# Optimization experiments

Hardware: AMD Instinct MI355X
Metric: run time of the kernel (lower is better)

## Reference

```python
import jax, jax.numpy as jnp
import numpy as np

B, N = 2, 6
C_IN, C_MID = 512, 512
D, C_OUT = 112, 80
OGH, OGW, DS = 256, 704, 16
FH, FW = OGH // DS, OGW // DS  # 16, 44
D_MIN, D_MAX = 2.0, 58.0
NX, NY, NZ = 128, 128, 1
VSIZE = np.array([0.8, 0.8, 8.0], dtype=np.float32)
VCOORD = np.array([-51.2 + 0.4, -51.2 + 0.4, -5.0 + 4.0], dtype=np.float32)


def make_frustum():
    # (D, FH, FW, 4) with entries (x_pix, y_pix, depth, 1)
    ones = jnp.ones((D, FH, FW), jnp.float32)
    d = jnp.linspace(D_MIN, D_MAX, D)[:, None, None] * jnp.ones((1, FH, FW))
    x = jnp.linspace(0.0, OGW - 1.0, FW)[None, None, :] * jnp.ones((D, FH, 1))
    y = jnp.linspace(0.0, OGH - 1.0, FH)[None, :, None] * jnp.ones((D, 1, FW))
    return jnp.stack([x, y, d, ones], axis=-1)


def setup_inputs() -> dict:
    key = jax.random.key(0)
    ks = jax.random.split(key, 24)
    eye = jnp.eye(4, dtype=jnp.float32)
    K = jnp.array([[1266.0, 0.0, 800.0, 0.0],
                   [0.0, 1266.0, 450.0, 0.0],
                   [0.0, 0.0, 1.0, 0.0],
                   [0.0, 0.0, 0.0, 1.0]], jnp.float32)
    inp = {
        'feat': jax.random.normal(ks[0], (B * N, C_IN, FH, FW), jnp.float32),
        'w1': 0.05 * jax.random.normal(ks[1], (C_MID, C_IN, 3, 3), jnp.float32),
        'g1': 1.0 + 0.1 * jax.random.normal(ks[2], (C_MID,), jnp.float32),
        'b1': 0.1 * jax.random.normal(ks[3], (C_MID,), jnp.float32),
        'm1': 0.1 * jax.random.normal(ks[4], (C_MID,), jnp.float32),
        'v1': 0.5 + jax.random.uniform(ks[5], (C_MID,), jnp.float32),
        'w2': 0.05 * jax.random.normal(ks[6], (C_MID, C_MID, 3, 3), jnp.float32),
        'g2': 1.0 + 0.1 * jax.random.normal(ks[7], (C_MID,), jnp.float32),
        'b2': 0.1 * jax.random.normal(ks[8], (C_MID,), jnp.float32),
        'm2': 0.1 * jax.random.normal(ks[9], (C_MID,), jnp.float32),
        'v2': 0.5 + jax.random.uniform(ks[10], (C_MID,), jnp.float32),
        'w_out': 0.05 * jax.random.normal(ks[11], (D + C_OUT, C_MID, 1, 1), jnp.float32),
        'b_out': 0.1 * jax.random.normal(ks[12], (D + C_OUT,), jnp.float32),
        'sensor2ego': eye + 0.05 * jax.random.normal(ks[13], (B, N, 4, 4), jnp.float32),
        'sensor2virtual': eye + 0.05 * jax.random.normal(ks[14], (B, N, 4, 4), jnp.float32),
        'intrin': K + 0.01 * jax.random.normal(ks[15], (B, N, 4, 4), jnp.float32),
        'ida': eye + 0.01 * jax.random.normal(ks[16], (B, N, 4, 4), jnp.float32),
        'ref_heights': 1.5 + 0.2 * jax.random.normal(ks[17], (B, N), jnp.float32),
        'bda': eye + 0.01 * jax.random.normal(ks[18], (B, 4, 4), jnp.float32),
    }
    return inp


def _conv(x, w, p):
    return jax.lax.conv_general_dilated(x, w, (1, 1), [(p, p), (p, p)],
                                         dimension_numbers=('NCHW', 'OIHW', 'NCHW'))


def _bn(x, g, b, m, v):
    s = (g / jnp.sqrt(v + 1e-5))
    return (x - m[None, :, None, None]) * s[None, :, None, None] + b[None, :, None, None]


def get_geometry(sensor2ego, sensor2virtual, intrin, ida, ref_heights, bda):
    frustum = make_frustum()[..., None]  # (D,FH,FW,4,1)
    pts = jnp.linalg.inv(ida)[:, :, None, None, None] @ frustum  # (B,N,D,FH,FW,4,1)
    ref = ref_heights[:, :, None, None, None, None]
    height = -pts[..., 2, :] + ref  # (B,N,D,FH,FW,1)
    pc = pts.at[..., 2, :].set(10.0)
    pc = jnp.concatenate([pc[..., :2, :] * pc[..., 2:3, :], pc[..., 2:, :]], axis=-2)
    cv = sensor2virtual @ jnp.linalg.inv(intrin)
    pv = cv[:, :, None, None, None] @ pc
    ratio = height[..., 0] / pv[..., 1, 0]  # (B,N,D,FH,FW)
    pts = pv * ratio[..., None, None]
    pts = pts.at[..., 3, :].set(1.0)
    ce = sensor2ego @ jnp.linalg.inv(sensor2virtual)
    pts = ce[:, :, None, None, None] @ pts
    pts = (bda[:, None, None, None, None] @ pts)[..., 0]
    return pts[..., :3]  # (B,N,D,FH,FW,3)


def reference(feat, w1, g1, b1, m1, v1, w2, g2, b2, m2, v2, w_out, b_out,
              sensor2ego, sensor2virtual, intrin, ida, ref_heights, bda):
    # DepthNet head
    h = jax.nn.relu(_bn(_conv(feat, w1, 1), g1, b1, m1, v1))
    h = jax.nn.relu(_bn(_conv(h, w2, 1), g2, b2, m2, v2))
    hf = _conv(h, w_out, 0) + b_out[None, :, None, None]  # (B*N, D+C, FH, FW)
    depth = jax.nn.softmax(hf[:, :D], axis=1).reshape(B, N, D, FH, FW)
    context = hf[:, D:].reshape(B, N, C_OUT, FH, FW)

    geom = get_geometry(sensor2ego, sensor2virtual, intrin, ida, ref_heights, bda)

    # voxel indices
    vsize = jnp.asarray(VSIZE)
    vcoord = jnp.asarray(VCOORD)
    idx = ((geom - (vcoord - vsize / 2.0)) / vsize).astype(jnp.int32)
    valid = (jnp.all(idx >= 0, axis=-1) & (idx[..., 0] < NX)
             & (idx[..., 1] < NY) & (idx[..., 2] < NZ))

    # LSS outer product: (B,N,D,FH,FW,C)
    vol = jnp.einsum('bndhw,bnchw->bndhwc', depth, context)
    YX = NY * NX
    sid = idx[..., 1] * NX + idx[..., 0] + jnp.arange(B, dtype=jnp.int32)[:, None, None, None, None] * YX
    sid = jnp.where(valid, sid, B * YX).reshape(-1)
    bev = jax.ops.segment_sum(vol.reshape(-1, C_OUT), sid, num_segments=B * YX + 1)[:B * YX]
    return bev.reshape(B, NY, NX, C_OUT).transpose(0, 3, 1, 2)  # (B,C,NY,NX)
```

## Files before the change

kernel.cpp:

```cpp
#include <hip/hip_runtime.h>
#include <stdint.h>

#define NB   2
#define NN   6
#define NIMG 12
#define CIN  512
#define CMID 512
#define DD   112
#define COUT 80
#define FHh  16
#define FWw  44
#define NPIX 704
#define NPOS 8448
#define KK   4608
#define NXg  128
#define NYg  128
#define YX   16384
#define MAT_STRIDE 56
#define PADPIX 828
#define PROW 46
#define KSPLIT 4
#define KCHUNK (KK/KSPLIT)
#define NSTEP (KCHUNK/32)

typedef short short8 __attribute__((ext_vector_type(8)));
typedef float f32x4  __attribute__((ext_vector_type(4)));

#define GLD16(g, l) __builtin_amdgcn_global_load_lds((const __attribute__((address_space(1))) void*)(g), (__attribute__((address_space(3))) void*)(l), 16, 0, 0)

__device__ __forceinline__ unsigned short f2bf(float f){
  unsigned u = __float_as_uint(f);
  u += 0x7fffu + ((u >> 16) & 1u);
  return (unsigned short)(u >> 16);
}
__device__ __forceinline__ float bf2f(unsigned short u){
  return __uint_as_float(((unsigned)u) << 16);
}

__device__ __forceinline__ f32x4 mfma16(short8 a, short8 b, f32x4 c){
  return __builtin_amdgcn_mfma_f32_16x16x32_bf16(a, b, c, 0, 0, 0);
}

#define N1 (CMID*KK)
__global__ void k_prep_misc(const float* __restrict__ w1, const float* __restrict__ w2,
                            const float* __restrict__ wout,
                            const float* __restrict__ g1, const float* __restrict__ b1,
                            const float* __restrict__ m1, const float* __restrict__ v1,
                            const float* __restrict__ g2, const float* __restrict__ b2,
                            const float* __restrict__ m2, const float* __restrict__ v2,
                            unsigned short* __restrict__ wb1, unsigned short* __restrict__ wb2,
                            unsigned short* __restrict__ wb3,
                            float* __restrict__ scale1, float* __restrict__ bias1,
                            float* __restrict__ scale2, float* __restrict__ bias2){
  int i = blockIdx.x*blockDim.x + threadIdx.x;
  if (i < 2*N1){
    const float* w = (i < N1) ? w1 : w2;
    unsigned short* wb = (i < N1) ? wb1 : wb2;
    int j = (i < N1) ? i : i - N1;
    int oc = j / KK; int jj = j - oc*KK;
    int r = jj >> 9; int ic = jj & 511;
    wb[j] = f2bf(w[(size_t)(oc*512 + ic)*9 + r]);
  } else if (i < 2*N1 + 192*CMID){
    int j = i - 2*N1;
    wb3[j] = f2bf(wout[j]);
  } else if (i < 2*N1 + 192*CMID + 512){
    int t = i - (2*N1 + 192*CMID);
    float s = g1[t] / sqrtf(v1[t] + 1e-5f);
    scale1[t] = s; bias1[t] = b1[t] - m1[t]*s;
  } else if (i < 2*N1 + 192*CMID + 1024){
    int t = i - (2*N1 + 192*CMID + 512);
    float s = g2[t] / sqrtf(v2[t] + 1e-5f);
    scale2[t] = s; bias2[t] = b2[t] - m2[t]*s;
  }
}

__global__ void k_zeropad(unsigned short* __restrict__ a, unsigned short* __restrict__ b,
                          float4* __restrict__ bev){
  int i = blockIdx.x*blockDim.x + threadIdx.x;
  if (i < NB*YX*COUT/4) bev[i] = make_float4(0.f,0.f,0.f,0.f);
  int img = i >> 16; int j = i & 65535;
  int seg = j >> 9, ch = j & 511;
  int pp;
  if (seg < 46)       pp = seg;
  else if (seg < 92)  pp = 17*PROW + (seg - 46);
  else { int s2 = seg - 92; int y = s2 >> 1; pp = y*PROW + ((s2 & 1) ? 45 : 0); }
  size_t off = (size_t)img*PADPIX*512 + (size_t)pp*512 + ch;
  a[off] = 0; b[off] = 0;
}

__global__ __launch_bounds__(256) void k_featpad(const float* __restrict__ feat,
                                                 unsigned short* __restrict__ dst){
  __shared__ float tile[32][65];
  int blk = blockIdx.x;
  int img = blk / 176; int r = blk - img*176;
  int cb = r / 11; int pb = r - cb*11;
  int c0 = cb*32, p0 = pb*64;
  int t = threadIdx.x;
  const float* s = feat + (size_t)img*CIN*NPIX + (size_t)c0*NPIX + p0;
  for (int ch = t>>6; ch < 32; ch += 4)
    tile[ch][t & 63] = s[(size_t)ch*NPIX + (t & 63)];
  __syncthreads();
  int ch = (t & 15)*2;
  for (int pix = t>>4; pix < 64; pix += 16){
    int p = p0 + pix;
    int y = p / FWw, x = p - y*FWw;
    unsigned v = (unsigned)f2bf(tile[ch][pix]) | ((unsigned)f2bf(tile[ch+1][pix]) << 16);
    *(unsigned*)(dst + (size_t)img*PADPIX*512 + ((y+1)*PROW + (x+1))*512 + c0 + ch) = v;
  }
}

__device__ void inv4(const double* A, double* out){
  double M[4][8];
  for (int i=0;i<4;i++){ for(int j=0;j<4;j++){ M[i][j]=A[i*4+j]; M[i][4+j]=(i==j)?1.0:0.0; } }
  for (int c=0;c<4;c++){
    int piv=c; double best=fabs(M[c][c]);
    for (int r=c+1;r<4;r++){ double a=fabs(M[r][c]); if(a>best){best=a;piv=r;} }
    if (piv!=c){ for(int j=0;j<8;j++){ double tt=M[c][j]; M[c][j]=M[piv][j]; M[piv][j]=tt; } }
    double inv = 1.0 / M[c][c];
    for (int j=0;j<8;j++) M[c][j]*=inv;
    for (int r=0;r<4;r++){ if(r==c) continue; double f=M[r][c];
      for (int j=0;j<8;j++) M[r][j]-=f*M[c][j]; }
  }
  for (int i=0;i<4;i++) for(int j=0;j<4;j++) out[i*4+j]=M[i][4+j];
}
__device__ void mm4(const double* A, const double* Bm, double* C){
  for (int i=0;i<4;i++) for(int j=0;j<4;j++){
    double s=0.0; for(int k=0;k<4;k++) s+=A[i*4+k]*Bm[k*4+j]; C[i*4+j]=s; }
}

__global__ void k_prep_mats(const float* __restrict__ s2e, const float* __restrict__ s2v,
                            const float* __restrict__ intr, const float* __restrict__ ida,
                            const float* __restrict__ refh, const float* __restrict__ bda,
                            double* __restrict__ mats){
  int t = threadIdx.x;
  if (t >= NIMG) return;
  int b = t / NN;
  double Mida[16], Ms2v[16], Mintr[16], Ms2e[16], Mbda[16];
  for (int i=0;i<16;i++){
    Mida[i] =(double)ida [t*16+i];
    Ms2v[i] =(double)s2v [t*16+i];
    Mintr[i]=(double)intr[t*16+i];
    Ms2e[i] =(double)s2e [t*16+i];
    Mbda[i] =(double)bda [b*16+i];
  }
  double* o = mats + (size_t)t*MAT_STRIDE;
  double tmp[16], tmp2[16];
  inv4(Mida, o);
  inv4(Mintr, tmp);  mm4(Ms2v, tmp, o+16);
  inv4(Ms2v, tmp);   mm4(Ms2e, tmp, tmp2);
  mm4(Mbda, tmp2, o+32);
  o[48] = (double)refh[t];
}

__global__ void k_geom(const double* __restrict__ mats, int* __restrict__ sid){
  int g = blockIdx.x*blockDim.x + threadIdx.x;
  int img = g / (DD*NPIX); int rem = g - img*(DD*NPIX);
  int d = rem / NPIX; int p = rem - d*NPIX;
  int h = p / FWw; int w = p - h*FWw;
  const double* M = mats + (size_t)img*MAT_STRIDE;
  float xf = (float)w * (703.0f/43.0f);
  float yf = (float)h * 17.0f;
  float df = 2.0f + (float)d * (56.0f/111.0f);
  double x = (double)xf, y = (double)yf, dep = (double)df;
  double p0 = M[0]*x + M[1]*y + M[2]*dep + M[3];
  double p1 = M[4]*x + M[5]*y + M[6]*dep + M[7];
  double p2 = M[8]*x + M[9]*y + M[10]*dep + M[11];
  double p3 = M[12]*x + M[13]*y + M[14]*dep + M[15];
  double height = M[48] - p2;
  double c0 = p0*10.0, c1 = p1*10.0, c2 = 10.0, c3 = p3;
  const double* C = M + 16;
  double q0 = C[0]*c0 + C[1]*c1 + C[2]*c2 + C[3]*c3;
  double q1 = C[4]*c0 + C[5]*c1 + C[6]*c2 + C[7]*c3;
  double q2 = C[8]*c0 + C[9]*c1 + C[10]*c2 + C[11]*c3;
  double ratio = height / q1;
  double r0 = q0*ratio, r1 = q1*ratio, r2 = q2*ratio, r3 = 1.0;
  const double* F = M + 32;
  double gx = F[0]*r0 + F[1]*r1 + F[2]*r2 + F[3]*r3;
  double gy = F[4]*r0 + F[5]*r1 + F[6]*r2 + F[7]*r3;
  double gz = F[8]*r0 + F[9]*r1 + F[10]*r2 + F[11]*r3;
  float gxf = (float)gx, gyf = (float)gy, gzf = (float)gz;
  const float vcx = (float)(-51.2 + 0.4);
  const float ox = vcx - 0.4f;
  const float oy = ox;
  const float oz = -1.0f - 4.0f;
  float tx = (gxf - ox) / 0.8f;
  float ty = (gyf - oy) / 0.8f;
  float tz = (gzf - oz) / 8.0f;
  int ix = (int)tx, iy = (int)ty, iz = (int)tz;
  bool valid = (tx==tx) && (ty==ty) && (tz==tz) &&
               (ix >= 0) && (ix < NXg) && (iy >= 0) && (iy < NYg) && (iz == 0);
  int b = img / NN;
  sid[g] = valid ? (b*YX + iy*NXg + ix) : -1;
}

__global__ __launch_bounds__(256, 4) void k_conv_sk(const unsigned short* __restrict__ W,
    const unsigned short* __restrict__ src, unsigned short* __restrict__ part){
  __shared__ __align__(16) short As[3][128*32];
  __shared__ __align__(16) short Bs[3][128*32];
  int t = threadIdx.x;
  int lane = t & 63, wv = t >> 6;
  int wm = wv >> 1, wn = wv & 1;
  int q = lane >> 4, ml = lane & 15;

  int id = blockIdx.x;
  int res = id & 7, slot = id >> 3;
  int g = res + 8*(slot >> 2);
  int mblk = slot & 3;
  int z = g / 66, n = g - z*66;
  int m0 = mblk*128, n0 = n*128, k0 = z*KCHUNK;

  int lrow = lane >> 2;
  int lcol = (lane & 3) * 8;
  const unsigned short* agp[2];
  const unsigned short* bgp[2];
  #pragma unroll
  for (int i=0;i<2;i++){
    int seg = wv*2 + i;
    agp[i] = W + (size_t)(m0 + seg*16 + lrow)*KK + lcol;
    int pos = n0 + seg*16 + lrow;
    int img = pos / NPIX; int p = pos - img*NPIX;
    int y = p / FWw; int x = p - y*FWw;
    bgp[i] = src + (size_t)img*PADPIX*512 + ((y+1)*PROW + (x+1))*512 + lcol;
  }

  f32x4 acc[4][4];
  #pragma unroll
  for (int i=0;i<4;i++)
    #pragma unroll
    for (int j=0;j<4;j++) acc[i][j] = (f32x4)0.0f;

  auto stage = [&](int step, int d){
    int kb = k0 + step*32;
    int r = kb >> 9;
    int ic0 = kb & 511;
    int r3 = r / 3;
    int koff = (r3*PROW + (r - r3*3))*512 + ic0 - (PROW+1)*512;
    #pragma unroll
    for (int i=0;i<2;i++){
      int seg = wv*2 + i;
      GLD16(agp[i] + kb,   (char*)As[d] + seg*1024);
      GLD16(bgp[i] + koff, (char*)Bs[d] + seg*1024);
    }
  };

  stage(0, 0); stage(1, 1);
  int d = 0;
  for (int k = 0; k < NSTEP; ++k){
    if (k < NSTEP-1) asm volatile("s_waitcnt vmcnt(4)" ::: "memory");
    else             asm volatile("s_waitcnt vmcnt(0)" ::: "memory");
    asm volatile("s_barrier" ::: "memory");
    if (k + 2 < NSTEP){
      int nxt = d + 2; if (nxt >= 3) nxt -= 3;
      stage(k + 2, nxt);
    }
    const short* Ab = As[d];
    const short* Bb = Bs[d];
    short8 fa[4], fb[4];
    #pragma unroll
    for (int mi=0;mi<4;mi++) fa[mi] = *(const short8*)(Ab + (wm*64 + mi*16 + ml)*32 + q*8);
    #pragma unroll
    for (int ni=0;ni<4;ni++) fb[ni] = *(const short8*)(Bb + (wn*64 + ni*16 + ml)*32 + q*8);
    #pragma unroll
    for (int mi=0;mi<4;mi++)
      #pragma unroll
      for (int ni=0;ni<4;ni++)
        acc[mi][ni] = mfma16(fb[ni], fa[mi], acc[mi][ni]);
    d = (d == 2) ? 0 : d + 1;
  }

  unsigned short* op = part + (size_t)z*NPOS*CMID;
  #pragma unroll
  for (int mi=0;mi<4;mi++){
    int oc = m0 + wm*64 + mi*16 + ml;
    #pragma unroll
    for (int ni=0;ni<4;ni++){
      f32x4 v = acc[mi][ni];
      #pragma unroll
      for (int rr=0;rr<4;rr++){
        int pos = n0 + wn*64 + ni*16 + q*4 + rr;
        op[(size_t)pos*CMID + oc] = f2bf(v[rr]);
      }
    }
  }
}

template<int OUT_PADDED>
__global__ void k_reduce(const unsigned short* __restrict__ part,
                         const float* __restrict__ scale, const float* __restrict__ bias,
                         unsigned short* __restrict__ out){
  int i2 = blockIdx.x*blockDim.x + threadIdx.x;
  int e0 = i2*2;
  const size_t S = (size_t)NPOS*CMID;
  unsigned p0 = *(const unsigned*)(part + e0);
  unsigned p1 = *(const unsigned*)(part + e0 + S);
  unsigned p2 = *(const unsigned*)(part + e0 + 2*S);
  unsigned p3 = *(const unsigned*)(part + e0 + 3*S);
  float s0 = bf2f((unsigned short)p0) + bf2f((unsigned short)p1)
           + bf2f((unsigned short)p2) + bf2f((unsigned short)p3);
  float s1 = bf2f((unsigned short)(p0>>16)) + bf2f((unsigned short)(p1>>16))
           + bf2f((unsigned short)(p2>>16)) + bf2f((unsigned short)(p3>>16));
  int pos = e0 >> 9, oc = e0 & 511;
  float v0 = fmaxf(s0*scale[oc]   + bias[oc],   0.0f);
  float v1 = fmaxf(s1*scale[oc+1] + bias[oc+1], 0.0f);
  unsigned packed = (unsigned)f2bf(v0) | ((unsigned)f2bf(v1) << 16);
  if (OUT_PADDED){
    int img = pos / NPIX; int p = pos - img*NPIX;
    int y = p / FWw; int x = p - y*FWw;
    *(unsigned*)(out + (size_t)img*PADPIX*512 + ((y+1)*PROW + (x+1))*512 + oc) = packed;
  } else {
    *(unsigned*)(out + e0) = packed;
  }
}

__global__ __launch_bounds__(256) void k_gemm64(const unsigned short* __restrict__ A,
    const unsigned short* __restrict__ Bt, const float* __restrict__ bout,
    float* __restrict__ hf){
  const int K = 512;
  __shared__ __align__(16) short As[64][32];
  __shared__ __align__(16) short Bs[128][32];
  int t = threadIdx.x;
  int m0 = blockIdx.x*64; int n0 = blockIdx.y*128;
  int lane = t & 63; int wv = t >> 6; int q = lane >> 4, ml = lane & 15;
  f32x4 acc[8];
  #pragma unroll
  for (int i=0;i<8;i++) acc[i] = (f32x4)0.0f;
  int ar = t >> 2, ac = (t & 3) * 8;
  int br = t >> 1, bc = (t & 1) * 16;
  const unsigned short* pa = A  + (size_t)(m0 + ar)*K + ac;
  const unsigned short* pb = Bt + (size_t)(n0 + br)*K + bc;
  for (int kb = 0; kb < K; kb += 32){
    uint4 av = *(const uint4*)(pa + kb);
    uint4 b0 = *(const uint4*)(pb + kb);
    uint4 b1 = *(const uint4*)(pb + kb + 8);
    __syncthreads();
    *(uint4*)&As[ar][ac] = av;
    *(uint4*)&Bs[br][bc] = b0; *(uint4*)&Bs[br][bc+8] = b1;
    __syncthreads();
    short8 fa = *(const short8*)&As[wv*16 + ml][q*8];
    #pragma unroll
    for (int ni=0;ni<8;ni++){
      short8 fb = *(const short8*)&Bs[ni*16 + ml][q*8];
      acc[ni] = mfma16(fb, fa, acc[ni]);
    }
  }
  int oc = m0 + wv*16 + ml;
  float bb = bout[oc];
  #pragma unroll
  for (int ni=0;ni<8;ni++)
    #pragma unroll
    for (int r=0;r<4;r++){
      int pos = n0 + ni*16 + q*4 + r;
      hf[(size_t)pos*192 + oc] = acc[ni][r] + bb;
    }
}

__global__ __launch_bounds__(128) void k_scatter(const float* __restrict__ hf,
                          const int* __restrict__ sidb, float* __restrict__ bev){
  int pos = blockIdx.x;
  int img = pos / NPIX; int p = pos - img*NPIX;
  __shared__ float sdep[DD];
  __shared__ int   ssid[DD];
  __shared__ float sctx[COUT];
  __shared__ float cwt[DD];
  __shared__ int   cvox[DD];
  __shared__ int   scnt;
  __shared__ float redm[2];
  __shared__ float reds[2];
  int t = threadIdx.x;
  int wv = t >> 6;
  if (t == 0) scnt = 0;
  const float* row = hf + (size_t)pos*192;
  float v = (t < DD) ? row[t] : -1e30f;
  for (int c = t; c < COUT; c += 128) sctx[c] = row[DD + c];
  if (t < DD) ssid[t] = sidb[(size_t)(img*DD + t)*NPIX + p];
  float m = v;
  #pragma unroll
  for (int o=32;o>=1;o>>=1) m = fmaxf(m, __shfl_xor(m, o, 64));
  if ((t & 63) == 0) redm[wv] = m;
  __syncthreads();
  float mx = fmaxf(redm[0], redm[1]);
  float e = (t < DD) ? __expf(v - mx) : 0.0f;
  float s = e;
  #pragma unroll
  for (int o=32;o>=1;o>>=1) s += __shfl_xor(s, o, 64);
  if ((t & 63) == 0) reds[wv] = s;
  __syncthreads();
  float inv = 1.0f / (reds[0] + reds[1]);
  if (t < DD) sdep[t] = e * inv;
  __syncthreads();
  if (t < DD){
    int sd = ssid[t];
    bool head = (sd >= 0) && (t == 0 || ssid[t-1] != sd);
    if (head){
      float w = 0.0f;
      for (int dd = t; dd < DD && ssid[dd] == sd; ++dd) w += sdep[dd];
      int i = atomicAdd(&scnt, 1);
      cvox[i] = sd; cwt[i] = w;
    }
  }
  __syncthreads();
  int H = scnt;
  for (int j = t; j < H*COUT; j += 128){
    int h = j / COUT, c = j - h*COUT;
    atomicAdd(&bev[(size_t)cvox[h]*COUT + c], cwt[h]*sctx[c]);
  }
}

__global__ __launch_bounds__(256) void k_transpose(const float* __restrict__ bev, float* __restrict__ out){
  __shared__ float tile[64*COUT];
  int blk = blockIdx.x;
  int b = blk >> 8; int yx0 = (blk & 255) * 64;
  int t = threadIdx.x;
  const float* src = bev + ((size_t)b*YX + yx0)*COUT;
  for (int j = t; j < 64*COUT; j += 256) tile[j] = src[j];
  __syncthreads();
  float* dst = out + (size_t)b*COUT*YX + yx0;
  for (int j = t; j < COUT*64; j += 256){
    int c = j >> 6, row = j & 63;
    dst[(size_t)c*YX + row] = tile[row*COUT + c];
  }
}

extern "C" void kernel_launch(void* const* d_in, const int* in_sizes, int n_in,
                              void* d_out, int out_size, void* d_ws, size_t ws_size,
                              hipStream_t stream) {
  const float* feat = (const float*)d_in[0];
  const float* w1   = (const float*)d_in[1];
  const float* g1   = (const float*)d_in[2];
  const float* b1   = (const float*)d_in[3];
  const float* m1   = (const float*)d_in[4];
  const float* v1   = (const float*)d_in[5];
  const float* w2   = (const float*)d_in[6];
  const float* g2   = (const float*)d_in[7];
  const float* b2   = (const float*)d_in[8];
  const float* m2   = (const float*)d_in[9];
  const float* v2   = (const float*)d_in[10];
  const float* wout = (const float*)d_in[11];
  const float* bout = (const float*)d_in[12];
  const float* s2e  = (const float*)d_in[13];
  const float* s2v  = (const float*)d_in[14];
  const float* intr = (const float*)d_in[15];
  const float* ida  = (const float*)d_in[16];
  const float* refh = (const float*)d_in[17];
  const float* bda  = (const float*)d_in[18];

  uint8_t* base = (uint8_t*)d_ws;
  size_t off = 0;
  auto alloc = [&](size_t bytes)->void*{
    void* r = base + off;
    off = (off + bytes + 255) & ~(size_t)255;
    return r;
  };
  unsigned short* wb1 = (unsigned short*)alloc((size_t)CMID*KK*2);
  unsigned short* wb2 = (unsigned short*)alloc((size_t)CMID*KK*2);
  unsigned short* wb3 = (unsigned short*)alloc((size_t)192*CMID*2);
  float* scale1 = (float*)alloc(CMID*4);
  float* bias1  = (float*)alloc(CMID*4);
  float* scale2 = (float*)alloc(CMID*4);
  float* bias2  = (float*)alloc(CMID*4);
  double* mats  = (double*)alloc((size_t)NIMG*MAT_STRIDE*8);

  size_t padded_bytes = (size_t)NIMG*PADPIX*512*2;
  uint8_t* regionE = (uint8_t*)alloc(padded_bytes);
  uint8_t* regionF = (uint8_t*)alloc(padded_bytes);
  int*   sid   = (int*)  alloc((size_t)NIMG*DD*NPIX*4);
  float* bev   = (float*)alloc((size_t)NB*YX*COUT*4);
  unsigned short* part = (unsigned short*)alloc((size_t)KSPLIT*NPOS*CMID*2);

  unsigned short* featpad = (unsigned short*)regionE;
  unsigned short* h2      = (unsigned short*)regionE;
  unsigned short* h1pad   = (unsigned short*)regionF;
  float*          hf      = (float*)regionF;

  int prep_n = 2*N1 + 192*CMID + 1024;
  k_prep_misc<<<(prep_n + 255)/256, 256, 0, stream>>>(w1, w2, wout, g1, b1, m1, v1,
      g2, b2, m2, v2, wb1, wb2, wb3, scale1, bias1, scale2, bias2);
  k_prep_mats<<<1, 64, 0, stream>>>(s2e, s2v, intr, ida, refh, bda, mats);
  k_geom<<<3696, 256, 0, stream>>>(mats, sid);

  k_zeropad<<<3072, 256, 0, stream>>>(featpad, h1pad, (float4*)bev);
  k_featpad<<<2112, 256, 0, stream>>>(feat, featpad);

  k_conv_sk<<<1056, 256, 0, stream>>>(wb1, featpad, part);
  k_reduce<1><<<NPOS*CMID/512, 256, 0, stream>>>(part, scale1, bias1, h1pad);
  k_conv_sk<<<1056, 256, 0, stream>>>(wb2, h1pad, part);
  k_reduce<0><<<NPOS*CMID/512, 256, 0, stream>>>(part, scale2, bias2, h2);
  k_gemm64<<<dim3(3, 66), 256, 0, stream>>>(wb3, h2, bout, hf);

  k_scatter<<<NPOS, 128, 0, stream>>>(hf, sid, bev);

  k_transpose<<<512, 256, 0, stream>>>(bev, (float*)d_out);
}
```

Measured before the change: 372.2 us.

## Raise conv split-K to 8 when workspace allows; double-buffer 1x1 GEMM with async LDS loads

```diff
diff --git a/kernel.cpp b/kernel.cpp
--- a/kernel.cpp
+++ b/kernel.cpp
@@ -19,9 +19,6 @@
 #define MAT_STRIDE 56
 #define PADPIX 828
 #define PROW 46
-#define KSPLIT 4
-#define KCHUNK (KK/KSPLIT)
-#define NSTEP (KCHUNK/32)
 
 typedef short short8 __attribute__((ext_vector_type(8)));
 typedef float f32x4  __attribute__((ext_vector_type(4)));
@@ -194,9 +191,10 @@
 }
 
 __global__ __launch_bounds__(256, 4) void k_conv_sk(const unsigned short* __restrict__ W,
-    const unsigned short* __restrict__ src, unsigned short* __restrict__ part){
-  __shared__ __align__(16) short As[3][128*32];
-  __shared__ __align__(16) short Bs[3][128*32];
+    const unsigned short* __restrict__ src, unsigned short* __restrict__ part,
+    int ksplit, int kchunk, int nstep){
+  __shared__ __align__(16) short As[2][128*32];
+  __shared__ __align__(16) short Bs[2][128*32];
   int t = threadIdx.x;
   int lane = t & 63, wv = t >> 6;
   int wm = wv >> 1, wn = wv & 1;
@@ -207,7 +205,7 @@
   int g = res + 8*(slot >> 2);
   int mblk = slot & 3;
   int z = g / 66, n = g - z*66;
-  int m0 = mblk*128, n0 = n*128, k0 = z*KCHUNK;
+  int m0 = mblk*128, n0 = n*128, k0 = z*kchunk;
 
   int lrow = lane >> 2;
   int lcol = (lane & 3) * 8;
@@ -229,8 +227,9 @@
     #pragma unroll
     for (int j=0;j<4;j++) acc[i][j] = (f32x4)0.0f;
 
-  auto stage = [&](int step, int d){
+  auto stage = [&](int step){
     int kb = k0 + step*32;
+    int d = step & 1;
     int r = kb >> 9;
     int ic0 = kb & 511;
     int r3 = r / 3;
@@ -243,18 +242,17 @@
     }
   };
 
-  stage(0, 0); stage(1, 1);
-  int d = 0;
-  for (int k = 0; k < NSTEP; ++k){
-    if (k < NSTEP-1) asm volatile("s_waitcnt vmcnt(4)" ::: "memory");
-    else             asm volatile("s_waitcnt vmcnt(0)" ::: "memory");
+  stage(0);
+  for (int k = 0; k < nstep; ++k){
+    if (k + 1 < nstep){
+      stage(k + 1);
+      asm volatile("s_waitcnt vmcnt(4)" ::: "memory");
+    } else {
+      asm volatile("s_waitcnt vmcnt(0)" ::: "memory");
+    }
     asm volatile("s_barrier" ::: "memory");
-    if (k + 2 < NSTEP){
-      int nxt = d + 2; if (nxt >= 3) nxt -= 3;
-      stage(k + 2, nxt);
-    }
-    const short* Ab = As[d];
-    const short* Bb = Bs[d];
+    const short* Ab = As[k & 1];
+    const short* Bb = Bs[k & 1];
     short8 fa[4], fb[4];
     #pragma unroll
     for (int mi=0;mi<4;mi++) fa[mi] = *(const short8*)(Ab + (wm*64 + mi*16 + ml)*32 + q*8);
@@ -265,7 +263,7 @@
       #pragma unroll
       for (int ni=0;ni<4;ni++)
         acc[mi][ni] = mfma16(fb[ni], fa[mi], acc[mi][ni]);
-    d = (d == 2) ? 0 : d + 1;
+    asm volatile("s_barrier" ::: "memory");
   }
 
   unsigned short* op = part + (size_t)z*NPOS*CMID;
@@ -287,18 +285,16 @@
 template<int OUT_PADDED>
 __global__ void k_reduce(const unsigned short* __restrict__ part,
                          const float* __restrict__ scale, const float* __restrict__ bias,
-                         unsigned short* __restrict__ out){
+                         unsigned short* __restrict__ out, int ksplit){
   int i2 = blockIdx.x*blockDim.x + threadIdx.x;
   int e0 = i2*2;
   const size_t S = (size_t)NPOS*CMID;
-  unsigned p0 = *(const unsigned*)(part + e0);
-  unsigned p1 = *(const unsigned*)(part + e0 + S);
-  unsigned p2 = *(const unsigned*)(part + e0 + 2*S);
-  unsigned p3 = *(const unsigned*)(part + e0 + 3*S);
-  float s0 = bf2f((unsigned short)p0) + bf2f((unsigned short)p1)
-           + bf2f((unsigned short)p2) + bf2f((unsigned short)p3);
-  float s1 = bf2f((unsigned short)(p0>>16)) + bf2f((unsigned short)(p1>>16))
-           + bf2f((unsigned short)(p2>>16)) + bf2f((unsigned short)(p3>>16));
+  float s0 = 0.0f, s1 = 0.0f;
+  for (int z = 0; z < ksplit; ++z){
+    unsigned pz = *(const unsigned*)(part + e0 + (size_t)z*S);
+    s0 += bf2f((unsigned short)pz);
+    s1 += bf2f((unsigned short)(pz >> 16));
+  }
   int pos = e0 >> 9, oc = e0 & 511;
   float v0 = fmaxf(s0*scale[oc]   + bias[oc],   0.0f);
   float v1 = fmaxf(s1*scale[oc+1] + bias[oc+1], 0.0f);
@@ -316,32 +312,48 @@
     const unsigned short* __restrict__ Bt, const float* __restrict__ bout,
     float* __restrict__ hf){
   const int K = 512;
-  __shared__ __align__(16) short As[64][32];
-  __shared__ __align__(16) short Bs[128][32];
+  __shared__ __align__(16) short As[2][64*32];
+  __shared__ __align__(16) short Bs[2][128*32];
   int t = threadIdx.x;
-  int m0 = blockIdx.x*64; int n0 = blockIdx.y*128;
-  int lane = t & 63; int wv = t >> 6; int q = lane >> 4, ml = lane & 15;
+  int lane = t & 63, wv = t >> 6;
+  int q = lane >> 4, ml = lane & 15;
+  int m0 = blockIdx.x*64, n0 = blockIdx.y*128;
+  int lrow = lane >> 2, lcol = (lane & 3) * 8;
+  const unsigned short* agp = A + (size_t)(m0 + wv*16 + lrow)*K + lcol;
+  const unsigned short* bgp[2];
+  #pragma unroll
+  for (int i=0;i<2;i++){
+    int seg = wv*2 + i;
+    bgp[i] = Bt + (size_t)(n0 + seg*16 + lrow)*K + lcol;
+  }
   f32x4 acc[8];
   #pragma unroll
   for (int i=0;i<8;i++) acc[i] = (f32x4)0.0f;
-  int ar = t >> 2, ac = (t & 3) * 8;
-  int br = t >> 1, bc = (t & 1) * 16;
-  const unsigned short* pa = A  + (size_t)(m0 + ar)*K + ac;
-  const unsigned short* pb = Bt + (size_t)(n0 + br)*K + bc;
-  for (int kb = 0; kb < K; kb += 32){
-    uint4 av = *(const uint4*)(pa + kb);
-    uint4 b0 = *(const uint4*)(pb + kb);
-    uint4 b1 = *(const uint4*)(pb + kb + 8);
-    __syncthreads();
-    *(uint4*)&As[ar][ac] = av;
-    *(uint4*)&Bs[br][bc] = b0; *(uint4*)&Bs[br][bc+8] = b1;
-    __syncthreads();
-    short8 fa = *(const short8*)&As[wv*16 + ml][q*8];
+
+  auto stage = [&](int s){
+    int d = s & 1; int kb = s*32;
+    GLD16(agp + kb, (char*)As[d] + wv*1024);
+    #pragma unroll
+    for (int i=0;i<2;i++)
+      GLD16(bgp[i] + kb, (char*)Bs[d] + (wv*2+i)*1024);
+  };
+
+  stage(0);
+  for (int k = 0; k < 16; ++k){
+    if (k < 15){
+      stage(k + 1);
+      asm volatile("s_waitcnt vmcnt(3)" ::: "memory");
+    } else {
+      asm volatile("s_waitcnt vmcnt(0)" ::: "memory");
+    }
+    asm volatile("s_barrier" ::: "memory");
+    short8 fa = *(const short8*)(As[k & 1] + (wv*16 + ml)*32 + q*8);
     #pragma unroll
     for (int ni=0;ni<8;ni++){
-      short8 fb = *(const short8*)&Bs[ni*16 + ml][q*8];
+      short8 fb = *(const short8*)(Bs[k & 1] + (ni*16 + ml)*32 + q*8);
       acc[ni] = mfma16(fb, fa, acc[ni]);
     }
+    asm volatile("s_barrier" ::: "memory");
   }
   int oc = m0 + wv*16 + ml;
   float bb = bout[oc];
@@ -465,7 +477,13 @@
   uint8_t* regionF = (uint8_t*)alloc(padded_bytes);
   int*   sid   = (int*)  alloc((size_t)NIMG*DD*NPIX*4);
   float* bev   = (float*)alloc((size_t)NB*YX*COUT*4);
-  unsigned short* part = (unsigned short*)alloc((size_t)KSPLIT*NPOS*CMID*2);
+
+  size_t slice = (size_t)NPOS*CMID*2;
+  size_t rem = (ws_size > off) ? ws_size - off : 0;
+  int ksplit = (rem >= 8*slice + 256) ? 8 : 4;
+  unsigned short* part = (unsigned short*)alloc((size_t)ksplit*slice);
+  int kchunk = KK / ksplit;
+  int nstep  = kchunk / 32;
 
   unsigned short* featpad = (unsigned short*)regionE;
   unsigned short* h2      = (unsigned short*)regionE;
@@ -481,10 +499,10 @@
   k_zeropad<<<3072, 256, 0, stream>>>(featpad, h1pad, (float4*)bev);
   k_featpad<<<2112, 256, 0, stream>>>(feat, featpad);
 
-  k_conv_sk<<<1056, 256, 0, stream>>>(wb1, featpad, part);
-  k_reduce<1><<<NPOS*CMID/512, 256, 0, stream>>>(part, scale1, bias1, h1pad);
-  k_conv_sk<<<1056, 256, 0, stream>>>(wb2, h1pad, part);
-  k_reduce<0><<<NPOS*CMID/512, 256, 0, stream>>>(part, scale2, bias2, h2);
+  k_conv_sk<<<264*ksplit, 256, 0, stream>>>(wb1, featpad, part, ksplit, kchunk, nstep);
+  k_reduce<1><<<NPOS*CMID/512, 256, 0, stream>>>(part, scale1, bias1, h1pad, ksplit);
+  k_conv_sk<<<264*ksplit, 256, 0, stream>>>(wb2, h1pad, part, ksplit, kchunk, nstep);
+  k_reduce<0><<<NPOS*CMID/512, 256, 0, stream>>>(part, scale2, bias2, h2, ksplit);
   k_gemm64<<<dim3(3, 66), 256, 0, stream>>>(wb3, h2, bout, hf);
 
   k_scatter<<<NPOS, 128, 0, stream>>>(hf, sid, bev);
```

New measurement: 371.9 us. About the same (-0.1%).
